# Performance work log

Measured on AMD Instinct MI355X. Metric: run time of the kernel, lower is better.

## Reference

```python
import jax, jax.numpy as jnp
import numpy as np

LAMBDA_SOFTMAX = 9.0   # opt.lambda_softmax
LAMBDA_LSE = 6.0       # opt.lambda_lse
MARGIN = 0.2
EPS = 1e-8


def setup_inputs() -> dict:
    key = jax.random.key(0)
    k1, k2, k3, k4 = jax.random.split(key, 4)
    N, F, W, D = 64, 64, 40, 512
    images = jax.random.normal(k1, (N, F, D), dtype=jnp.float32)
    captions = jax.random.normal(k2, (N, W, D), dtype=jnp.float32)
    img_lens = jax.random.randint(k3, (N,), F // 2, F + 1)
    cap_lens = jax.random.randint(k4, (N,), W // 2, W + 1)
    return {"images": images, "captions": captions,
            "img_lens": img_lens, "cap_lens": cap_lens}


def _xattn_scores(images, captions, img_lens, cap_lens):
    # images: (N, F, D) queries; captions: (N, W, D) contexts
    N, F, D = images.shape
    W = captions.shape[1]
    fmask = jnp.arange(F)[None, :] < img_lens[:, None]   # (N_img, F)
    wmask = jnp.arange(W)[None, :] < cap_lens[:, None]   # (N_cap, W)
    # raw attention for every (caption j, image i) pair: (j, i, w, f)
    A = jnp.einsum('jwd,ifd->jiwf', captions, images)
    pair_mask = wmask[:, None, :, None] & fmask[None, :, None, :]
    A = jnp.where(pair_mask, A, 0.0)
    # clipped_l2norm: LeakyReLU(0.1) then l2-normalize along frame axis
    A = jnp.where(A > 0, A, 0.1 * A)
    A = A / (jnp.sqrt(jnp.sum(A * A, axis=3, keepdims=True)) + EPS)
    # softmax over words (sourceL) with temperature lambda_softmax
    logits = jnp.swapaxes(A, 2, 3) * LAMBDA_SOFTMAX       # (j, i, f, w)
    logits = jnp.where(wmask[:, None, None, :], logits, -jnp.inf)
    aw = jax.nn.softmax(logits, axis=-1)                  # (j, i, f, w)
    # weighted context per frame: (j, i, f, d)
    wctx = jnp.einsum('jifw,jwd->jifd', aw, captions)
    # per-frame cosine similarity between image frame and weighted context
    num = jnp.einsum('ifd,jifd->jif', images, wctx)
    n1 = jnp.linalg.norm(images, axis=-1)                 # (i, f)
    n2 = jnp.linalg.norm(wctx, axis=-1)                   # (j, i, f)
    sim = num / jnp.maximum(n1[None, :, :] * n2, EPS)     # (j, i, f)
    # LogSumExp aggregation over valid frames (unstabilized, as in torch)
    e = jnp.exp(sim * LAMBDA_LSE) * fmask[None, :, :]
    scores = jnp.log(jnp.sum(e, axis=-1)) / LAMBDA_LSE    # (n_cap, n_img)
    return scores


def reference(images, captions, img_lens, cap_lens):
    S = _xattn_scores(images, captions, img_lens, cap_lens)  # (N, N)
    diag = jnp.diagonal(S)
    eye = jnp.eye(S.shape[0], dtype=bool)
    cost_s = jnp.maximum(MARGIN + S - diag[:, None], 0.0)
    cost_im = jnp.maximum(MARGIN + S - diag[None, :], 0.0)
    cost_s = jnp.where(eye, 0.0, cost_s)
    cost_im = jnp.where(eye, 0.0, cost_im)
    # max_violation=True: hardest negative per row/col
    return jnp.max(cost_s, axis=1).sum() + jnp.max(cost_im, axis=0).sum()
```

## Files before the change

kernel.cpp:

```cpp
#include <hip/hip_runtime.h>
#include <math.h>

#define N 64
#define F 64
#define W 40
#define D 512
#define LSM 9.0f
#define LLSE 6.0f
#define MARG 0.2f
#define ESTR 56

typedef _Float16 f16x8 __attribute__((ext_vector_type(8)));
typedef _Float16 f16x4 __attribute__((ext_vector_type(4)));
typedef float f32x4 __attribute__((ext_vector_type(4)));

__device__ inline void gll16(const void* g, void* l) {
  __builtin_amdgcn_global_load_lds(
      (const __attribute__((address_space(1))) unsigned int*)g,
      (__attribute__((address_space(3))) unsigned int*)l, 16, 0, 0);
}


__global__ __launch_bounds__(512) void k_pre(
    const float* __restrict__ img, const float* __restrict__ cap,
    _Float16* __restrict__ img_h, _Float16* __restrict__ cap_h,
    _Float16* __restrict__ G_h, float* __restrict__ n1) {
  __shared__ __align__(16) _Float16 capT[4 * 48 * 128];
  int t = threadIdx.x;
  int b = blockIdx.x;
  if (b < 256) {
    int i = b >> 2;
    int f = ((b & 3) << 4) + (t >> 5);
    int q = t & 31;
    const float* row = img + ((size_t)i * F + f) * D + q * 16;
    _Float16* dsti = img_h + (size_t)i * 32768;
    int fsw = (f & 7) << 3;
    float s = 0.f;
    int d0 = q * 16;
    int ch = d0 >> 6, din = d0 & 63;
#pragma unroll
    for (int k = 0; k < 2; ++k) {
      float4 u = *(const float4*)(row + k * 8);
      float4 v = *(const float4*)(row + k * 8 + 4);
      s += u.x * u.x + u.y * u.y + u.z * u.z + u.w * u.w;
      s += v.x * v.x + v.y * v.y + v.z * v.z + v.w * v.w;
      f16x8 h;
      h[0] = (_Float16)u.x; h[1] = (_Float16)u.y; h[2] = (_Float16)u.z; h[3] = (_Float16)u.w;
      h[4] = (_Float16)v.x; h[5] = (_Float16)v.y; h[6] = (_Float16)v.z; h[7] = (_Float16)v.w;
      *(f16x8*)(dsti + ch * 4096 + f * 64 + ((din + k * 8) ^ fsw)) = h;
    }
    s += __shfl_xor(s, 1);
    s += __shfl_xor(s, 2);
    s += __shfl_xor(s, 4);
    s += __shfl_xor(s, 8);
    s += __shfl_xor(s, 16);
    if (q == 0) n1[i * F + f] = sqrtf(s);
  } else {
    int j = b - 256;
    int lane = t & 63, wv = t >> 6;
    const float* src = cap + (size_t)j * W * D;
    _Float16* dst = cap_h + (size_t)j * 24576;
#pragma unroll
    for (int k = 0; k < 6; ++k) {
      int slot = t + k * 512;
      int w = slot >> 6, d = (slot & 63) * 8;
      float4 u = {0.f, 0.f, 0.f, 0.f}, v = {0.f, 0.f, 0.f, 0.f};
      if (w < W) {
        u = *(const float4*)(src + (size_t)w * D + d);
        v = *(const float4*)(src + (size_t)w * D + d + 4);
      }
      f16x8 h;
      h[0] = (_Float16)u.x; h[1] = (_Float16)u.y; h[2] = (_Float16)u.z; h[3] = (_Float16)u.w;
      h[4] = (_Float16)v.x; h[5] = (_Float16)v.y; h[6] = (_Float16)v.z; h[7] = (_Float16)v.w;
      int wsw = (w & 7) << 3;
      int ch2 = d >> 6, din2 = d & 63;
      *(f16x8*)(dst + ch2 * 3072 + w * 64 + (din2 ^ wsw)) = h;
      int chO = d >> 7, dinO = d & 127;
      *(f16x8*)(capT + chO * 6144 + w * 128 + (dinO ^ wsw)) = h;
    }
    __syncthreads();
    int lane2 = t & 63;
    int rlo = lane2 & 15, hi = lane2 >> 4;
    int koff = hi * 8, sw = (rlo & 7) << 3;
    _Float16* gb = G_h + (size_t)j * 3072;
    for (int tile = wv; tile < 9; tile += 8) {
      int mt = tile / 3, kt = tile % 3;
      f32x4 acc = (f32x4)0.f;
#pragma unroll
      for (int ks = 0; ks < 16; ++ks) {
        int kk = ks * 32 + koff;
        int ch = kk >> 7, din = (kk & 127) ^ sw;
        f16x8 af = *(const f16x8*)(capT + ch * 6144 + (mt * 16 + rlo) * 128 + din);
        f16x8 bf = *(const f16x8*)(capT + ch * 6144 + (kt * 16 + rlo) * 128 + din);
        acc = __builtin_amdgcn_mfma_f32_16x16x32_f16(af, bf, acc, 0, 0, 0);
      }
#pragma unroll
      for (int r = 0; r < 4; ++r) {
        int w = mt * 16 + hi * 4 + r, k = kt * 16 + rlo;
        float val = (w < W && k < W) ? acc[r] : 0.f;
        gb[w * 64 + k] = (_Float16)val;
      }
    }
    if (t < 96) {
      int w = t >> 1, c8 = 48 + (t & 1) * 8;
      *(f16x8*)(gb + w * 64 + c8) = (f16x8)(_Float16)0.f;
    }
  }
}

__global__ __launch_bounds__(512, 2) void k_fused(
    const _Float16* __restrict__ img_h, const _Float16* __restrict__ cap_h,
    const int* __restrict__ imgL, const int* __restrict__ capL,
    const float* __restrict__ n1g, const _Float16* __restrict__ G_h,
    float* __restrict__ S) {
  __shared__ __align__(16) char buf[114688];

  int t = threadIdx.x;
  int lane = t & 63, wv = t >> 6;
  int rlo = lane & 15, hi = lane >> 4;
  int koff = hi * 8;
  int sw = (rlo & 7) << 3;
  int wm = wv >> 2, wn = wv & 3;

  int bid = blockIdx.x;
  int xcd = bid & 7, s0 = bid >> 3;
  int bj = (xcd & 3) * 4 + (s0 & 3);
  int bi = (xcd >> 2) * 8 + (s0 >> 2);

  int i = bi * 4 + wn;
  int ja = bj * 4 + wm * 2;
  int iL = imgL[i];
  int cLa = capL[ja], cLb = capL[ja + 1];

  const char* capb = (const char*)cap_h + (size_t)bj * 4 * 49152;
  const char* imgb = (const char*)img_h + (size_t)bi * 4 * 65536;

  const char* bsrc[7];
  int cstr[7], mdst[7];
#pragma unroll
  for (int s = 0; s < 7; ++s) {
    int m = s * 8 + wv;
    if (m < 24) {
      bsrc[s] = capb + (m / 6) * 49152 + (m % 6) * 1024 + lane * 16;
      cstr[s] = 6144;
    } else {
      int e = m - 24;
      bsrc[s] = imgb + (e >> 3) * 65536 + (e & 7) * 1024 + lane * 16;
      cstr[s] = 8192;
    }
    mdst[s] = m * 1024;
  }

  f32x4 acc[6][4];
#pragma unroll
  for (int mt = 0; mt < 6; ++mt)
#pragma unroll
    for (int nt = 0; nt < 4; ++nt) acc[mt][nt] = (f32x4)0.f;

#pragma unroll
  for (int s = 0; s < 7; ++s) gll16(bsrc[s], buf + mdst[s]);

#pragma unroll
  for (int c = 0; c < 8; ++c) {
    if (c < 7) {
      char* db = buf + ((c + 1) & 1) * 57344;
#pragma unroll
      for (int s = 0; s < 7; ++s) gll16(bsrc[s] + (c + 1) * cstr[s], db + mdst[s]);
      asm volatile("s_waitcnt vmcnt(7)" ::: "memory");
    } else {
      asm volatile("s_waitcnt vmcnt(0)" ::: "memory");
    }
    __builtin_amdgcn_s_barrier();
    __builtin_amdgcn_sched_barrier(0);
    const char* cb = buf + (c & 1) * 57344;
    const _Float16* Al = (const _Float16*)cb;
    const _Float16* Bl = (const _Float16*)(cb + 24576) + wn * 4096;
#pragma unroll
    for (int ks = 0; ks < 2; ++ks) {
      int col = (ks * 32 + koff) ^ sw;
      f16x8 bf[4], af[6];
#pragma unroll
      for (int nt = 0; nt < 4; ++nt) bf[nt] = *(const f16x8*)(Bl + (nt * 16 + rlo) * 64 + col);
#pragma unroll
      for (int mt = 0; mt < 6; ++mt) {
        int blk = wm * 2 + (mt >= 3 ? 1 : 0);
        int w = (mt >= 3 ? mt - 3 : mt) * 16 + rlo;
        af[mt] = *(const f16x8*)(Al + blk * 3072 + w * 64 + col);
      }
      __builtin_amdgcn_s_setprio(1);
#pragma unroll
      for (int mt = 0; mt < 6; ++mt)
#pragma unroll
        for (int nt = 0; nt < 4; ++nt)
          acc[mt][nt] = __builtin_amdgcn_mfma_f32_16x16x32_f16(af[mt], bf[nt], acc[mt][nt], 0, 0, 0);
      __builtin_amdgcn_s_setprio(0);
    }
    __builtin_amdgcn_sched_barrier(0);
    __builtin_amdgcn_s_barrier();
  }

  _Float16* Ew = (_Float16*)(buf + wv * 7168);
  float n1lane = n1g[i * F + lane];

#pragma unroll
  for (int p = 0; p < 2; ++p) {
    int j = ja + p;
    int cL = p ? cLb : cLa;
    int mb = p * 3;

    float rinv[3][4];
#pragma unroll
    for (int mt = 0; mt < 3; ++mt)
#pragma unroll
      for (int r = 0; r < 4; ++r) {
        float s = 0.f;
#pragma unroll
        for (int nt = 0; nt < 4; ++nt) {
          float a = acc[mb + mt][nt][r];
          float l = a > 0.f ? a : 0.1f * a;
          s += ((nt * 16 + rlo) < iL) ? l * l : 0.f;
        }
#pragma unroll
        for (int d = 1; d < 16; d <<= 1) s += __shfl_xor(s, d);
        rinv[mt][r] = 1.f / (sqrtf(s) + 1e-8f);
      }

    float sn[4] = {0.f, 0.f, 0.f, 0.f};
    f16x4 evs[3][4];
#pragma unroll
    for (int mt = 0; mt < 3; ++mt)
#pragma unroll
      for (int nt = 0; nt < 4; ++nt) {
        f16x4 ev;
#pragma unroll
        for (int r = 0; r < 4; ++r) {
          int w = mt * 16 + hi * 4 + r;
          float a = acc[mb + mt][nt][r];
          float l = a > 0.f ? a : 0.1f * a;
          float e = (w < cL) ? __expf(LSM * l * rinv[mt][r]) : 0.f;
          sn[nt] = fmaf(e, a, sn[nt]);
          ev[r] = (_Float16)e;
        }
        evs[mt][nt] = ev;
        *(f16x4*)(Ew + (nt * 16 + rlo) * ESTR + mt * 16 + hi * 4) = ev;
      }
#pragma unroll
    for (int nt = 0; nt < 4; ++nt) {
      sn[nt] += __shfl_xor(sn[nt], 16);
      sn[nt] += __shfl_xor(sn[nt], 32);
    }

    const _Float16* gB = G_h + (size_t)j * 3072;
    f32x4 P2[3][4];
#pragma unroll
    for (int wb = 0; wb < 3; ++wb)
#pragma unroll
      for (int fb = 0; fb < 4; ++fb) P2[wb][fb] = (f32x4)0.f;
#pragma unroll
    for (int ks2 = 0; ks2 < 2; ++ks2) {
      int kk2 = ks2 * 32 + koff;
      f16x8 ga[3], eb[4];
#pragma unroll
      for (int wb = 0; wb < 3; ++wb)
        ga[wb] = *(const f16x8*)(gB + (wb * 16 + rlo) * 64 + kk2);
#pragma unroll
      for (int fb = 0; fb < 4; ++fb)
        eb[fb] = *(const f16x8*)(Ew + (fb * 16 + rlo) * ESTR + kk2);
#pragma unroll
      for (int wb = 0; wb < 3; ++wb)
#pragma unroll
        for (int fb = 0; fb < 4; ++fb)
          P2[wb][fb] = __builtin_amdgcn_mfma_f32_16x16x32_f16(ga[wb], eb[fb], P2[wb][fb], 0, 0, 0);
    }

    float ef = 0.f;
#pragma unroll
    for (int fb = 0; fb < 4; ++fb) {
      int f = fb * 16 + rlo;
      float n2s = 0.f;
#pragma unroll
      for (int wb = 0; wb < 3; ++wb)
#pragma unroll
        for (int r = 0; r < 4; ++r)
          n2s = fmaf(P2[wb][fb][r], (float)evs[wb][fb][r], n2s);
      n2s += __shfl_xor(n2s, 16);
      n2s += __shfl_xor(n2s, 32);
      float nm = sn[fb];
      float n1v = __shfl(n1lane, f);
      float denom = n1v * sqrtf(fmaxf(n2s, 0.f));
      float sim = nm / fmaxf(denom, 1e-20f);
      ef += (f < iL) ? __expf(LLSE * sim) : 0.f;
    }
    ef += __shfl_xor(ef, 1);
    ef += __shfl_xor(ef, 2);
    ef += __shfl_xor(ef, 4);
    ef += __shfl_xor(ef, 8);
    if (lane == 0) S[(j << 6) + i] = __logf(ef) * (1.f / LLSE);
  }
}

__global__ void k_loss(const float* __restrict__ S, float* __restrict__ out) {
  __shared__ float red[128];
  int t = threadIdx.x;
  float m = -1e30f;
  if (t < 64) {
    int a = t;
    float da = S[a * N + a];
    for (int b = 0; b < N; ++b)
      if (b != a) m = fmaxf(m, MARG + S[a * N + b] - da);
  } else {
    int b = t - 64;
    float db = S[b * N + b];
    for (int a = 0; a < N; ++a)
      if (a != b) m = fmaxf(m, MARG + S[a * N + b] - db);
  }
  red[t] = fmaxf(m, 0.f);
  __syncthreads();
  if (t < 64) {
    float v = red[t] + red[t + 64];
#pragma unroll
    for (int off = 1; off < 64; off <<= 1) v += __shfl_xor(v, off);
    if (t == 0) *out = v;
  }
}

extern "C" void kernel_launch(void* const* d_in, const int* in_sizes, int n_in,
                              void* d_out, int out_size, void* d_ws, size_t ws_size,
                              hipStream_t stream) {
  const float* img = (const float*)d_in[0];
  const float* cap = (const float*)d_in[1];
  const int* imgL = (const int*)d_in[2];
  const int* capL = (const int*)d_in[3];

  char* wsb = (char*)d_ws;
  float* n1 = (float*)wsb;
  float* S = (float*)(wsb + 16384);
  _Float16* img_h = (_Float16*)(wsb + 32768);
  _Float16* cap_h = (_Float16*)(wsb + 32768 + 4194304);
  _Float16* G_h = (_Float16*)(wsb + 32768 + 4194304 + 3145728);

  k_pre<<<320, 512, 0, stream>>>(img, cap, img_h, cap_h, G_h, n1);
  k_fused<<<256, 512, 0, stream>>>(img_h, cap_h, imgL, capL, n1, G_h, S);
  k_loss<<<1, 128, 0, stream>>>(S, (float*)d_out);
}
```

Measured before the change: 48.04 us.

## Shrink fused block tile to 4 captions x 2 images, load image operands directly

The fused kernel now tiles 4 captions by 2 images per block instead of 4x4, with each wave handling one (caption, image) pair. It launches 512 blocks and targets 4 blocks per CU with half the LDS. Image operands are read straight from global memory into registers, and only caption tiles are staged through LDS. The goal is higher occupancy and more blocks to hide latency. The cost is less image data reuse across waves and more global traffic per MFMA.

```diff
diff --git a/kernel.cpp b/kernel.cpp
--- a/kernel.cpp
+++ b/kernel.cpp
@@ -108,91 +108,84 @@
   }
 }
 
-__global__ __launch_bounds__(512, 2) void k_fused(
+__global__ __launch_bounds__(512, 4) void k_fused(
     const _Float16* __restrict__ img_h, const _Float16* __restrict__ cap_h,
     const int* __restrict__ imgL, const int* __restrict__ capL,
     const float* __restrict__ n1g, const _Float16* __restrict__ G_h,
     float* __restrict__ S) {
-  __shared__ __align__(16) char buf[114688];
+  __shared__ __align__(16) char buf[57600];
 
   int t = threadIdx.x;
   int lane = t & 63, wv = t >> 6;
   int rlo = lane & 15, hi = lane >> 4;
   int koff = hi * 8;
   int sw = (rlo & 7) << 3;
-  int wm = wv >> 2, wn = wv & 3;
+  int wm = wv >> 1, wn = wv & 1;
 
   int bid = blockIdx.x;
   int xcd = bid & 7, s0 = bid >> 3;
-  int bj = (xcd & 3) * 4 + (s0 & 3);
-  int bi = (xcd >> 2) * 8 + (s0 >> 2);
-
-  int i = bi * 4 + wn;
-  int ja = bj * 4 + wm * 2;
-  int iL = imgL[i];
-  int cLa = capL[ja], cLb = capL[ja + 1];
-
-  const char* capb = (const char*)cap_h + (size_t)bj * 4 * 49152;
-  const char* imgb = (const char*)img_h + (size_t)bi * 4 * 65536;
-
-  const char* bsrc[7];
-  int cstr[7], mdst[7];
-#pragma unroll
-  for (int s = 0; s < 7; ++s) {
+  int mt = (xcd & 1) * 8 + (s0 & 7);
+  int nt2 = (xcd >> 1) * 8 + (s0 >> 3);
+  int j = mt * 4 + wm;
+  int i = nt2 * 2 + wn;
+
+  int iL = imgL[i], cL = capL[j];
+
+  const char* capb = (const char*)cap_h + (size_t)mt * 4 * 49152;
+  const _Float16* ibase = img_h + (size_t)i * 32768;
+
+  const char* bsrc[3];
+  int mdst[3];
+#pragma unroll
+  for (int s = 0; s < 3; ++s) {
     int m = s * 8 + wv;
-    if (m < 24) {
-      bsrc[s] = capb + (m / 6) * 49152 + (m % 6) * 1024 + lane * 16;
-      cstr[s] = 6144;
+    bsrc[s] = capb + (m / 6) * 49152 + (m % 6) * 1024 + lane * 16;
+    mdst[s] = m * 1024;
+  }
+
+  f32x4 acc[3][4];
+#pragma unroll
+  for (int mtl = 0; mtl < 3; ++mtl)
+#pragma unroll
+    for (int nt = 0; nt < 4; ++nt) acc[mtl][nt] = (f32x4)0.f;
+
+#pragma unroll
+  for (int s = 0; s < 3; ++s) gll16(bsrc[s], buf + mdst[s]);
+
+#pragma unroll
+  for (int c = 0; c < 8; ++c) {
+    f16x8 bf[8];
+#pragma unroll
+    for (int ks = 0; ks < 2; ++ks)
+#pragma unroll
+      for (int nt = 0; nt < 4; ++nt)
+        bf[ks * 4 + nt] =
+            *(const f16x8*)(ibase + c * 4096 + (nt * 16 + rlo) * 64 + ((ks * 32 + koff) ^ sw));
+    if (c < 7) {
+      char* db = buf + ((c + 1) & 1) * 24576;
+#pragma unroll
+      for (int s = 0; s < 3; ++s) gll16(bsrc[s] + (c + 1) * 6144, db + mdst[s]);
+      asm volatile("s_waitcnt vmcnt(11)" ::: "memory");
     } else {
-      int e = m - 24;
-      bsrc[s] = imgb + (e >> 3) * 65536 + (e & 7) * 1024 + lane * 16;
-      cstr[s] = 8192;
-    }
-    mdst[s] = m * 1024;
-  }
-
-  f32x4 acc[6][4];
-#pragma unroll
-  for (int mt = 0; mt < 6; ++mt)
-#pragma unroll
-    for (int nt = 0; nt < 4; ++nt) acc[mt][nt] = (f32x4)0.f;
-
-#pragma unroll
-  for (int s = 0; s < 7; ++s) gll16(bsrc[s], buf + mdst[s]);
-
-#pragma unroll
-  for (int c = 0; c < 8; ++c) {
-    if (c < 7) {
-      char* db = buf + ((c + 1) & 1) * 57344;
-#pragma unroll
-      for (int s = 0; s < 7; ++s) gll16(bsrc[s] + (c + 1) * cstr[s], db + mdst[s]);
-      asm volatile("s_waitcnt vmcnt(7)" ::: "memory");
-    } else {
-      asm volatile("s_waitcnt vmcnt(0)" ::: "memory");
+      asm volatile("s_waitcnt vmcnt(8)" ::: "memory");
     }
     __builtin_amdgcn_s_barrier();
     __builtin_amdgcn_sched_barrier(0);
-    const char* cb = buf + (c & 1) * 57344;
-    const _Float16* Al = (const _Float16*)cb;
-    const _Float16* Bl = (const _Float16*)(cb + 24576) + wn * 4096;
+    const char* cb = buf + (c & 1) * 24576;
 #pragma unroll
     for (int ks = 0; ks < 2; ++ks) {
-      int col = (ks * 32 + koff) ^ sw;
-      f16x8 bf[4], af[6];
-#pragma unroll
-      for (int nt = 0; nt < 4; ++nt) bf[nt] = *(const f16x8*)(Bl + (nt * 16 + rlo) * 64 + col);
-#pragma unroll
-      for (int mt = 0; mt < 6; ++mt) {
-        int blk = wm * 2 + (mt >= 3 ? 1 : 0);
-        int w = (mt >= 3 ? mt - 3 : mt) * 16 + rlo;
-        af[mt] = *(const f16x8*)(Al + blk * 3072 + w * 64 + col);
-      }
+      int col2 = (((ks * 32 + koff) ^ sw)) * 2;
+      f16x8 af[3];
+#pragma unroll
+      for (int mtl = 0; mtl < 3; ++mtl)
+        af[mtl] = *(const f16x8*)(cb + wm * 6144 + (mtl * 16 + rlo) * 128 + col2);
       __builtin_amdgcn_s_setprio(1);
 #pragma unroll
-      for (int mt = 0; mt < 6; ++mt)
+      for (int mtl = 0; mtl < 3; ++mtl)
 #pragma unroll
         for (int nt = 0; nt < 4; ++nt)
-          acc[mt][nt] = __builtin_amdgcn_mfma_f32_16x16x32_f16(af[mt], bf[nt], acc[mt][nt], 0, 0, 0);
+          acc[mtl][nt] =
+              __builtin_amdgcn_mfma_f32_16x16x32_f16(af[mtl], bf[ks * 4 + nt], acc[mtl][nt], 0, 0, 0);
       __builtin_amdgcn_s_setprio(0);
     }
     __builtin_amdgcn_sched_barrier(0);
@@ -200,103 +193,102 @@
   }
 
   _Float16* Ew = (_Float16*)(buf + wv * 7168);
+#pragma unroll
+  for (int z = 0; z < 7; ++z)
+    *(f16x8*)(buf + wv * 7168 + (z * 64 + lane) * 16) = (f16x8)(_Float16)0.f;
+  if (wv == 7 && lane < 16)
+    *(f16x8*)(buf + 57344 + lane * 16) = (f16x8)(_Float16)0.f;
+
   float n1lane = n1g[i * F + lane];
 
-#pragma unroll
-  for (int p = 0; p < 2; ++p) {
-    int j = ja + p;
-    int cL = p ? cLb : cLa;
-    int mb = p * 3;
-
-    float rinv[3][4];
-#pragma unroll
-    for (int mt = 0; mt < 3; ++mt)
+  float rinv[3][4];
+#pragma unroll
+  for (int mtl = 0; mtl < 3; ++mtl)
+#pragma unroll
+    for (int r = 0; r < 4; ++r) {
+      float s = 0.f;
+#pragma unroll
+      for (int nt = 0; nt < 4; ++nt) {
+        float a = acc[mtl][nt][r];
+        float l = a > 0.f ? a : 0.1f * a;
+        s += ((nt * 16 + rlo) < iL) ? l * l : 0.f;
+      }
+#pragma unroll
+      for (int d = 1; d < 16; d <<= 1) s += __shfl_xor(s, d);
+      rinv[mtl][r] = 1.f / (sqrtf(s) + 1e-8f);
+    }
+
+  float sn[4] = {0.f, 0.f, 0.f, 0.f};
+  f16x4 evs[3][4];
+#pragma unroll
+  for (int mtl = 0; mtl < 3; ++mtl)
+#pragma unroll
+    for (int nt = 0; nt < 4; ++nt) {
+      f16x4 ev;
 #pragma unroll
       for (int r = 0; r < 4; ++r) {
-        float s = 0.f;
-#pragma unroll
-        for (int nt = 0; nt < 4; ++nt) {
-          float a = acc[mb + mt][nt][r];
-          float l = a > 0.f ? a : 0.1f * a;
-          s += ((nt * 16 + rlo) < iL) ? l * l : 0.f;
-        }
-#pragma unroll
-        for (int d = 1; d < 16; d <<= 1) s += __shfl_xor(s, d);
-        rinv[mt][r] = 1.f / (sqrtf(s) + 1e-8f);
-      }
-
-    float sn[4] = {0.f, 0.f, 0.f, 0.f};
-    f16x4 evs[3][4];
-#pragma unroll
-    for (int mt = 0; mt < 3; ++mt)
-#pragma unroll
-      for (int nt = 0; nt < 4; ++nt) {
-        f16x4 ev;
-#pragma unroll
-        for (int r = 0; r < 4; ++r) {
-          int w = mt * 16 + hi * 4 + r;
-          float a = acc[mb + mt][nt][r];
-          float l = a > 0.f ? a : 0.1f * a;
-          float e = (w < cL) ? __expf(LSM * l * rinv[mt][r]) : 0.f;
-          sn[nt] = fmaf(e, a, sn[nt]);
-          ev[r] = (_Float16)e;
-        }
-        evs[mt][nt] = ev;
-        *(f16x4*)(Ew + (nt * 16 + rlo) * ESTR + mt * 16 + hi * 4) = ev;
-      }
-#pragma unroll
-    for (int nt = 0; nt < 4; ++nt) {
-      sn[nt] += __shfl_xor(sn[nt], 16);
-      sn[nt] += __shfl_xor(sn[nt], 32);
-    }
-
-    const _Float16* gB = G_h + (size_t)j * 3072;
-    f32x4 P2[3][4];
+        int w = mtl * 16 + hi * 4 + r;
+        float a = acc[mtl][nt][r];
+        float l = a > 0.f ? a : 0.1f * a;
+        float e = (w < cL) ? __expf(LSM * l * rinv[mtl][r]) : 0.f;
+        sn[nt] = fmaf(e, a, sn[nt]);
+        ev[r] = (_Float16)e;
+      }
+      evs[mtl][nt] = ev;
+      *(f16x4*)(Ew + (nt * 16 + rlo) * ESTR + mtl * 16 + hi * 4) = ev;
+    }
+#pragma unroll
+  for (int nt = 0; nt < 4; ++nt) {
+    sn[nt] += __shfl_xor(sn[nt], 16);
+    sn[nt] += __shfl_xor(sn[nt], 32);
+  }
+
+  const _Float16* gB = G_h + (size_t)j * 3072;
+  f32x4 P2[3][4];
+#pragma unroll
+  for (int wb = 0; wb < 3; ++wb)
+#pragma unroll
+    for (int fb = 0; fb < 4; ++fb) P2[wb][fb] = (f32x4)0.f;
+#pragma unroll
+  for (int ks2 = 0; ks2 < 2; ++ks2) {
+    int kk2 = ks2 * 32 + koff;
+    f16x8 ga[3], eb[4];
 #pragma unroll
     for (int wb = 0; wb < 3; ++wb)
-#pragma unroll
-      for (int fb = 0; fb < 4; ++fb) P2[wb][fb] = (f32x4)0.f;
-#pragma unroll
-    for (int ks2 = 0; ks2 < 2; ++ks2) {
-      int kk2 = ks2 * 32 + koff;
-      f16x8 ga[3], eb[4];
-#pragma unroll
-      for (int wb = 0; wb < 3; ++wb)
-        ga[wb] = *(const f16x8*)(gB + (wb * 16 + rlo) * 64 + kk2);
+      ga[wb] = *(const f16x8*)(gB + (wb * 16 + rlo) * 64 + kk2);
+#pragma unroll
+    for (int fb = 0; fb < 4; ++fb)
+      eb[fb] = *(const f16x8*)(Ew + (fb * 16 + rlo) * ESTR + kk2);
+#pragma unroll
+    for (int wb = 0; wb < 3; ++wb)
 #pragma unroll
       for (int fb = 0; fb < 4; ++fb)
-        eb[fb] = *(const f16x8*)(Ew + (fb * 16 + rlo) * ESTR + kk2);
-#pragma unroll
-      for (int wb = 0; wb < 3; ++wb)
-#pragma unroll
-        for (int fb = 0; fb < 4; ++fb)
-          P2[wb][fb] = __builtin_amdgcn_mfma_f32_16x16x32_f16(ga[wb], eb[fb], P2[wb][fb], 0, 0, 0);
-    }
-
-    float ef = 0.f;
-#pragma unroll
-    for (int fb = 0; fb < 4; ++fb) {
-      int f = fb * 16 + rlo;
-      float n2s = 0.f;
-#pragma unroll
-      for (int wb = 0; wb < 3; ++wb)
-#pragma unroll
-        for (int r = 0; r < 4; ++r)
-          n2s = fmaf(P2[wb][fb][r], (float)evs[wb][fb][r], n2s);
-      n2s += __shfl_xor(n2s, 16);
-      n2s += __shfl_xor(n2s, 32);
-      float nm = sn[fb];
-      float n1v = __shfl(n1lane, f);
-      float denom = n1v * sqrtf(fmaxf(n2s, 0.f));
-      float sim = nm / fmaxf(denom, 1e-20f);
-      ef += (f < iL) ? __expf(LLSE * sim) : 0.f;
-    }
-    ef += __shfl_xor(ef, 1);
-    ef += __shfl_xor(ef, 2);
-    ef += __shfl_xor(ef, 4);
-    ef += __shfl_xor(ef, 8);
-    if (lane == 0) S[(j << 6) + i] = __logf(ef) * (1.f / LLSE);
-  }
+        P2[wb][fb] = __builtin_amdgcn_mfma_f32_16x16x32_f16(ga[wb], eb[fb], P2[wb][fb], 0, 0, 0);
+  }
+
+  float ef = 0.f;
+#pragma unroll
+  for (int fb = 0; fb < 4; ++fb) {
+    int f = fb * 16 + rlo;
+    float n2s = 0.f;
+#pragma unroll
+    for (int wb = 0; wb < 3; ++wb)
+#pragma unroll
+      for (int r = 0; r < 4; ++r)
+        n2s = fmaf(P2[wb][fb][r], (float)evs[wb][fb][r], n2s);
+    n2s += __shfl_xor(n2s, 16);
+    n2s += __shfl_xor(n2s, 32);
+    float nm = sn[fb];
+    float n1v = __shfl(n1lane, f);
+    float denom = n1v * sqrtf(fmaxf(n2s, 0.f));
+    float sim = nm / fmaxf(denom, 1e-20f);
+    ef += (f < iL) ? __expf(LLSE * sim) : 0.f;
+  }
+  ef += __shfl_xor(ef, 1);
+  ef += __shfl_xor(ef, 2);
+  ef += __shfl_xor(ef, 4);
+  ef += __shfl_xor(ef, 8);
+  if (lane == 0) S[(j << 6) + i] = __logf(ef) * (1.f / LLSE);
 }
 
 __global__ void k_loss(const float* __restrict__ S, float* __restrict__ out) {
@@ -340,6 +332,6 @@
   _Float16* G_h = (_Float16*)(wsb + 32768 + 4194304 + 3145728);
 
   k_pre<<<320, 512, 0, stream>>>(img, cap, img_h, cap_h, G_h, n1);
-  k_fused<<<256, 512, 0, stream>>>(img_h, cap_h, imgL, capL, n1, G_h, S);
+  k_fused<<<512, 512, 0, stream>>>(img_h, cap_h, imgL, capL, n1, G_h, S);
   k_loss<<<1, 128, 0, stream>>>(S, (float*)d_out);
 }
```

Result: slower. 57.07 us (+18.8%).
